# Optimization experiments

Measured on AMD Instinct MI355X. Metric: run time of the kernel, lower is better.

The kernel has to match this reference:

```python
import jax, jax.numpy as jnp
import numpy as np

N_NODES = 50000
N_EDGES = 800000
IN_DIM = 64
HID = 128
NUM_LAYERS = 4
N_GRAPHS = 1024
LEAKY_SLOPE = 0.01


def setup_inputs() -> dict:
    key = jax.random.key(0)
    ks = jax.random.split(key, 16)
    s = 0.05
    inp = {
        "x": jax.random.normal(ks[0], (N_NODES, IN_DIM), dtype=jnp.float32),
        "edge_index": jax.random.randint(ks[1], (2, N_EDGES), 0, N_NODES, dtype=jnp.int64),
        "batch": jnp.sort(jax.random.randint(ks[2], (N_NODES,), 0, N_GRAPHS, dtype=jnp.int64)),
        # layer 0 (in=IN_DIM -> HID, residual projection)
        "l0_W1": jax.random.normal(ks[3], (IN_DIM, HID), dtype=jnp.float32) * s,
        "l0_b1": jnp.zeros((HID,), jnp.float32),
        "l0_W2": jax.random.normal(ks[4], (HID, HID), dtype=jnp.float32) * s,
        "l0_b2": jnp.zeros((HID,), jnp.float32),
        "l0_Wres": jax.random.normal(ks[5], (IN_DIM, HID), dtype=jnp.float32) * s,
        # layers 1..NUM_LAYERS-1 (HID -> HID, identity residual), stacked
        "Ws1": jax.random.normal(ks[6], (NUM_LAYERS - 1, HID, HID), dtype=jnp.float32) * s,
        "bs1": jnp.zeros((NUM_LAYERS - 1, HID), jnp.float32),
        "Ws2": jax.random.normal(ks[7], (NUM_LAYERS - 1, HID, HID), dtype=jnp.float32) * s,
        "bs2": jnp.zeros((NUM_LAYERS - 1, HID), jnp.float32),
        # fc head
        "fW1": jax.random.normal(ks[8], (HID, HID), dtype=jnp.float32) * s,
        "fb1": jnp.zeros((HID,), jnp.float32),
        "fW2": jax.random.normal(ks[9], (HID, 1), dtype=jnp.float32) * s,
        "fb2": jnp.zeros((1,), jnp.float32),
    }
    return inp


def _gin_layer(x, src, dst, W1, b1, W2, b2, res):
    # GIN sum aggregation: gather source node features, scatter-add at targets
    agg = jax.ops.segment_sum(x[src], dst, num_segments=N_NODES)  # [N, d]
    h = x + agg  # (1 + eps) * x + agg, eps = 0
    h = jax.nn.relu(h @ W1 + b1) @ W2 + b2
    return jax.nn.relu(h + res)


def reference(x, edge_index, batch,
              l0_W1, l0_b1, l0_W2, l0_b2, l0_Wres,
              Ws1, bs1, Ws2, bs2,
              fW1, fb1, fW2, fb2):
    src, dst = edge_index[0], edge_index[1]
    # layer 0 with linear residual projection (in_dim != hidden_dim)
    h = _gin_layer(x, src, dst, l0_W1, l0_b1, l0_W2, l0_b2, x @ l0_Wres)
    # remaining layers with identity residual
    for i in range(NUM_LAYERS - 1):
        h = _gin_layer(h, src, dst, Ws1[i], bs1[i], Ws2[i], bs2[i], h)
    # global mean pool over graphs
    sums = jax.ops.segment_sum(h, batch, num_segments=N_GRAPHS)  # [G, HID]
    counts = jax.ops.segment_sum(jnp.ones((h.shape[0],), h.dtype), batch, num_segments=N_GRAPHS)
    pooled = sums / jnp.maximum(counts, 1.0)[:, None]
    # fc head: Linear -> LeakyReLU -> Linear
    out = jax.nn.leaky_relu(pooled @ fW1 + fb1, negative_slope=LEAKY_SLOPE) @ fW2 + fb2
    return out  # [G, 1]
```

## Files before the change

kernel.cpp:

```cpp
#include <hip/hip_runtime.h>

#define NN 50000
#define NE 800000
#define IND 64
#define HID 128
#define NG 1024

#define NBK 391
#define BCAP 2560

typedef short bf16x8 __attribute__((ext_vector_type(8)));
typedef float f32x4 __attribute__((ext_vector_type(4)));

static __device__ __forceinline__ unsigned short f2bf(float f) {
    unsigned int u = __float_as_uint(f);
    return (unsigned short)((u + 0x7FFFu + ((u >> 16) & 1u)) >> 16);
}
static __device__ __forceinline__ float bf2f(unsigned short h) {
    return __uint_as_float(((unsigned int)h) << 16);
}
static __device__ __forceinline__ float4 f4zero() { return make_float4(0.f, 0.f, 0.f, 0.f); }

__global__ void bin_kernel(const int* __restrict__ src, const int* __restrict__ dst,
                           int* __restrict__ bcur, unsigned int* __restrict__ bedge) {
    __shared__ int hist[NBK];
    __shared__ int base[NBK];
    int tid = threadIdx.x;
    for (int i = tid; i < NBK; i += 256) hist[i] = 0;
    __syncthreads();
    int e0 = blockIdx.x * 4096;
    unsigned int pk[16];
    int bk[16], lo[16];
#pragma unroll
    for (int j = 0; j < 16; ++j) {
        int e = e0 + j * 256 + tid;
        bk[j] = -1;
        if (e < NE) {
            int s = src[e], d = dst[e];
            pk[j] = (unsigned int)s | ((unsigned int)d << 16);
            bk[j] = d >> 7;
            lo[j] = atomicAdd(&hist[bk[j]], 1);
        }
    }
    __syncthreads();
    for (int i = tid; i < NBK; i += 256)
        base[i] = hist[i] ? atomicAdd(&bcur[i], hist[i]) : 0;
    __syncthreads();
#pragma unroll
    for (int j = 0; j < 16; ++j) {
        if (bk[j] >= 0) {
            int idx = base[bk[j]] + lo[j];
            if (idx < BCAP) bedge[(size_t)bk[j] * BCAP + idx] = pk[j];
        }
    }
}

__global__ void build_csr_kernel(const unsigned int* __restrict__ bedge,
                                 const int* __restrict__ bcur, int* __restrict__ row_beg,
                                 int* __restrict__ row_end, int* __restrict__ esrc) {
    __shared__ unsigned int se[BCAP];
    __shared__ int h[128], sc[128], cur[128];
    int b = blockIdx.x, tid = threadIdx.x;
    int cnt = min(bcur[b], BCAP);
    for (int i = tid; i < cnt; i += 256) se[i] = bedge[(size_t)b * BCAP + i];
    if (tid < 128) h[tid] = 0;
    __syncthreads();
    for (int i = tid; i < cnt; i += 256) atomicAdd(&h[(se[i] >> 16) & 127], 1);
    __syncthreads();
    if (tid < 128) sc[tid] = h[tid];
    __syncthreads();
    for (int off = 1; off < 128; off <<= 1) {
        int add = 0;
        if (tid < 128 && tid >= off) add = sc[tid - off];
        __syncthreads();
        if (tid < 128) sc[tid] += add;
        __syncthreads();
    }
    if (tid < 128) {
        int ex = sc[tid] - h[tid];
        int n = (b << 7) + tid;
        if (n < NN) {
            row_beg[n] = b * BCAP + ex;
            row_end[n] = b * BCAP + sc[tid];
        }
        cur[tid] = ex;
    }
    __syncthreads();
    for (int i = tid; i < cnt; i += 256) {
        unsigned int v = se[i];
        int dl = (v >> 16) & 127;
        int pos = atomicAdd(&cur[dl], 1);
        esrc[(size_t)b * BCAP + pos] = (int)(v & 0xffffu);
    }
}

__global__ void convert_all(const float* __restrict__ Wres, const float* __restrict__ W1,
                            const float* __restrict__ W2, const float* __restrict__ Ws1,
                            const float* __restrict__ Ws2, short* __restrict__ wresHi,
                            short* __restrict__ wresLo, short* __restrict__ w1Hi,
                            short* __restrict__ w1Lo, short* __restrict__ w2Hi,
                            short* __restrict__ w2Lo, short* __restrict__ ws1Hi,
                            short* __restrict__ ws1Lo, short* __restrict__ ws2Hi,
                            short* __restrict__ ws2Lo) {
    int t = blockIdx.x * 256 + threadIdx.x;
    const float* W;
    short *hi, *lo;
    int K, idx;
    if (t < 8192) { W = Wres; hi = wresHi; lo = wresLo; K = 64; idx = t; }
    else if (t < 16384) { W = W1; hi = w1Hi; lo = w1Lo; K = 64; idx = t - 8192; }
    else if (t < 32768) { W = W2; hi = w2Hi; lo = w2Lo; K = 128; idx = t - 16384; }
    else if (t < 81920) { W = Ws1; hi = ws1Hi; lo = ws1Lo; K = 128; idx = t - 32768; }
    else { W = Ws2; hi = ws2Hi; lo = ws2Lo; K = 128; idx = t - 81920; }
    int m = idx / (K * 128);
    int r = idx - m * K * 128;
    int n = r / K, k = r - n * K;
    float w = W[(size_t)m * K * 128 + k * 128 + n];
    unsigned short hh = f2bf(w);
    hi[idx] = (short)hh;
    lo[idx] = (short)f2bf(w - bf2f(hh));
}

__global__ void to_bf16_kernel(const float* __restrict__ s, short* __restrict__ d, int total) {
    int i = blockIdx.x * 256 + threadIdx.x;
    if (i < total) d[i] = (short)f2bf(s[i]);
}

__global__ void agg128b_kernel(const unsigned int* __restrict__ hb, const float* __restrict__ hf,
                               const int* __restrict__ row_beg, const int* __restrict__ row_end,
                               const int* __restrict__ es, float* __restrict__ t) {
    int wv = threadIdx.x >> 6, lane = threadIdx.x & 63;
    int n = blockIdx.x * 4 + wv;
    if (n >= NN) return;
    int beg = row_beg[n], end = row_end[n];
    float2 acc = ((const float2*)hf)[(size_t)n * 64 + lane];
    int e = beg;
    for (; e + 8 <= end; e += 8) {
        unsigned int v0 = hb[(size_t)es[e] * 64 + lane];
        unsigned int v1 = hb[(size_t)es[e + 1] * 64 + lane];
        unsigned int v2 = hb[(size_t)es[e + 2] * 64 + lane];
        unsigned int v3 = hb[(size_t)es[e + 3] * 64 + lane];
        unsigned int v4 = hb[(size_t)es[e + 4] * 64 + lane];
        unsigned int v5 = hb[(size_t)es[e + 5] * 64 + lane];
        unsigned int v6 = hb[(size_t)es[e + 6] * 64 + lane];
        unsigned int v7 = hb[(size_t)es[e + 7] * 64 + lane];
        acc.x += __uint_as_float(v0 << 16) + __uint_as_float(v1 << 16) +
                 __uint_as_float(v2 << 16) + __uint_as_float(v3 << 16) +
                 __uint_as_float(v4 << 16) + __uint_as_float(v5 << 16) +
                 __uint_as_float(v6 << 16) + __uint_as_float(v7 << 16);
        acc.y += __uint_as_float(v0 & 0xffff0000u) + __uint_as_float(v1 & 0xffff0000u) +
                 __uint_as_float(v2 & 0xffff0000u) + __uint_as_float(v3 & 0xffff0000u) +
                 __uint_as_float(v4 & 0xffff0000u) + __uint_as_float(v5 & 0xffff0000u) +
                 __uint_as_float(v6 & 0xffff0000u) + __uint_as_float(v7 & 0xffff0000u);
    }
    for (; e + 4 <= end; e += 4) {
        unsigned int v0 = hb[(size_t)es[e] * 64 + lane];
        unsigned int v1 = hb[(size_t)es[e + 1] * 64 + lane];
        unsigned int v2 = hb[(size_t)es[e + 2] * 64 + lane];
        unsigned int v3 = hb[(size_t)es[e + 3] * 64 + lane];
        acc.x += __uint_as_float(v0 << 16) + __uint_as_float(v1 << 16) +
                 __uint_as_float(v2 << 16) + __uint_as_float(v3 << 16);
        acc.y += __uint_as_float(v0 & 0xffff0000u) + __uint_as_float(v1 & 0xffff0000u) +
                 __uint_as_float(v2 & 0xffff0000u) + __uint_as_float(v3 & 0xffff0000u);
    }
    for (; e < end; ++e) {
        unsigned int v = hb[(size_t)es[e] * 64 + lane];
        acc.x += __uint_as_float(v << 16);
        acc.y += __uint_as_float(v & 0xffff0000u);
    }
    ((float2*)t)[(size_t)n * 64 + lane] = acc;
}

__global__ void agg64b_kernel(const unsigned short* __restrict__ xb, const float* __restrict__ xf,
                              const int* __restrict__ row_beg, const int* __restrict__ row_end,
                              const int* __restrict__ es, float* __restrict__ t) {
    int wv = threadIdx.x >> 6, lane = threadIdx.x & 63;
    int n = blockIdx.x * 4 + wv;
    if (n >= NN) return;
    int beg = row_beg[n], end = row_end[n];
    float acc = xf[(size_t)n * 64 + lane];
    int e = beg;
    for (; e + 4 <= end; e += 4) {
        int s0 = es[e], s1 = es[e + 1], s2 = es[e + 2], s3 = es[e + 3];
        acc += bf2f(xb[(size_t)s0 * 64 + lane]) + bf2f(xb[(size_t)s1 * 64 + lane]) +
               bf2f(xb[(size_t)s2 * 64 + lane]) + bf2f(xb[(size_t)s3 * 64 + lane]);
    }
    for (; e < end; ++e) acc += bf2f(xb[(size_t)es[e] * 64 + lane]);
    t[(size_t)n * 64 + lane] = acc;
}

__global__ __launch_bounds__(256, 3) void fused2(
    const float* __restrict__ tin, const float* __restrict__ xres,
    const short* __restrict__ W1Hi, const short* __restrict__ W1Lo,
    const float* __restrict__ b1, const short* __restrict__ W2Hi,
    const short* __restrict__ W2Lo, const float* __restrict__ b2,
    float* __restrict__ hout, short* __restrict__ hbout) {
    __shared__ short lds[16384];
    int tid = threadIdx.x;
    int rowBase = blockIdx.x * 64;
    int lane = tid & 63, wv = tid >> 6;
    int m = lane & 15, g = lane >> 4;

    float4 sv[8];
#pragma unroll
    for (int j = 0; j < 8; ++j) {
        int i = j * 256 + tid;
        int r = i >> 5, c4 = i & 31;
        int row = rowBase + r;
        sv[j] = f4zero();
        if (row < NN) sv[j] = ((const float4*)(tin + (size_t)row * 128))[c4];
    }
    bf16x8 wh[2][4], wl[2][4];
#pragma unroll
    for (int ctl = 0; ctl < 2; ++ctl) {
        int col = wv * 32 + ctl * 16 + m;
#pragma unroll
        for (int kc = 0; kc < 4; ++kc) {
            wh[ctl][kc] = *(const bf16x8*)(W1Hi + col * 128 + kc * 32 + g * 8);
            wl[ctl][kc] = *(const bf16x8*)(W1Lo + col * 128 + kc * 32 + g * 8);
        }
    }
#pragma unroll
    for (int j = 0; j < 8; ++j) {
        int i = j * 256 + tid;
        int r = i >> 5, c4 = i & 31;
        float4 v = sv[j];
        unsigned short hx = f2bf(v.x), hy = f2bf(v.y), hz = f2bf(v.z), hw = f2bf(v.w);
        short4 hv = {(short)hx, (short)hy, (short)hz, (short)hw};
        short4 lv = {(short)f2bf(v.x - bf2f(hx)), (short)f2bf(v.y - bf2f(hy)),
                     (short)f2bf(v.z - bf2f(hz)), (short)f2bf(v.w - bf2f(hw))};
        int sidx = (r * 128 + c4 * 4) ^ ((r & 7) << 3);
        *(short4*)(lds + sidx) = hv;
        *(short4*)(lds + 8192 + sidx) = lv;
    }
    __syncthreads();

    f32x4 acc1[4][2];
#pragma unroll
    for (int s = 0; s < 4; ++s) {
        int rloc = s * 16 + m;
        bf16x8 tHi[4], tLo[4];
#pragma unroll
        for (int kc = 0; kc < 4; ++kc) {
            int idx = (rloc * 128 + kc * 32 + g * 8) ^ ((rloc & 7) << 3);
            tHi[kc] = *(const bf16x8*)(lds + idx);
            tLo[kc] = *(const bf16x8*)(lds + 8192 + idx);
        }
#pragma unroll
        for (int ctl = 0; ctl < 2; ++ctl) {
            float bv = b1[wv * 32 + ctl * 16 + m];
            f32x4 a = {bv, bv, bv, bv};
#pragma unroll
            for (int kc = 0; kc < 4; ++kc) {
                a = __builtin_amdgcn_mfma_f32_16x16x32_bf16(tHi[kc], wh[ctl][kc], a, 0, 0, 0);
                a = __builtin_amdgcn_mfma_f32_16x16x32_bf16(tLo[kc], wh[ctl][kc], a, 0, 0, 0);
                a = __builtin_amdgcn_mfma_f32_16x16x32_bf16(tHi[kc], wl[ctl][kc], a, 0, 0, 0);
            }
            acc1[s][ctl] = a;
        }
    }
    __syncthreads();

#pragma unroll
    for (int s = 0; s < 4; ++s) {
#pragma unroll
        for (int ctl = 0; ctl < 2; ++ctl) {
            int col = wv * 32 + ctl * 16 + m;
#pragma unroll
            for (int i = 0; i < 4; ++i) {
                float u = fmaxf(acc1[s][ctl][i], 0.f);
                unsigned short uh = f2bf(u);
                int ru = s * 16 + g * 4 + i;
                int sidx = (ru * 128 + col) ^ ((ru & 7) << 3);
                lds[sidx] = (short)uh;
                lds[8192 + sidx] = (short)f2bf(u - bf2f(uh));
            }
        }
    }
#pragma unroll
    for (int ctl = 0; ctl < 2; ++ctl) {
        int col = wv * 32 + ctl * 16 + m;
#pragma unroll
        for (int kc = 0; kc < 4; ++kc) {
            wh[ctl][kc] = *(const bf16x8*)(W2Hi + col * 128 + kc * 32 + g * 8);
            wl[ctl][kc] = *(const bf16x8*)(W2Lo + col * 128 + kc * 32 + g * 8);
        }
    }
    __syncthreads();

#pragma unroll
    for (int s = 0; s < 4; ++s) {
        int rloc = s * 16 + m;
        bf16x8 uHi[4], uLo[4];
#pragma unroll
        for (int kc = 0; kc < 4; ++kc) {
            int idx = (rloc * 128 + kc * 32 + g * 8) ^ ((rloc & 7) << 3);
            uHi[kc] = *(const bf16x8*)(lds + idx);
            uLo[kc] = *(const bf16x8*)(lds + 8192 + idx);
        }
#pragma unroll
        for (int ctl = 0; ctl < 2; ++ctl) {
            int col = wv * 32 + ctl * 16 + m;
            float bv = b2[col];
            f32x4 a = {bv, bv, bv, bv};
#pragma unroll
            for (int kc = 0; kc < 4; ++kc) {
                a = __builtin_amdgcn_mfma_f32_16x16x32_bf16(uHi[kc], wh[ctl][kc], a, 0, 0, 0);
                a = __builtin_amdgcn_mfma_f32_16x16x32_bf16(uLo[kc], wh[ctl][kc], a, 0, 0, 0);
                a = __builtin_amdgcn_mfma_f32_16x16x32_bf16(uHi[kc], wl[ctl][kc], a, 0, 0, 0);
            }
#pragma unroll
            for (int i = 0; i < 4; ++i) {
                int row = rowBase + s * 16 + g * 4 + i;
                if (row < NN) {
                    float v = fmaxf(a[i] + xres[(size_t)row * 128 + col], 0.f);
                    hout[(size_t)row * 128 + col] = v;
                    hbout[(size_t)row * 128 + col] = (short)f2bf(v);
                }
            }
        }
    }
}

template <int L0>
__global__ __launch_bounds__(256, 4) void fused_layer(
    const float* __restrict__ tin, const float* __restrict__ xres,
    const short* __restrict__ W1Hi, const short* __restrict__ W1Lo,
    const float* __restrict__ b1, const short* __restrict__ W2Hi,
    const short* __restrict__ W2Lo, const float* __restrict__ b2,
    const short* __restrict__ WrHi, const short* __restrict__ WrLo,
    float* __restrict__ hout, short* __restrict__ hbout) {
    constexpr int KIN = L0 ? 64 : 128;
    constexpr int NKC1 = KIN / 32;
    __shared__ short lds[16384];
    int tid = threadIdx.x;
    int rowBase = blockIdx.x * 64;
    int lane = tid & 63, wv = tid >> 6;
    int m = lane & 15, g = lane >> 4;

    for (int i = tid; i < 64 * KIN / 4; i += 256) {
        int r = i / (KIN / 4), c4 = i - r * (KIN / 4);
        int row = rowBase + r;
        float4 v = f4zero();
        if (row < NN) v = ((const float4*)(tin + (size_t)row * KIN))[c4];
        unsigned short hx = f2bf(v.x), hy = f2bf(v.y), hz = f2bf(v.z), hw = f2bf(v.w);
        short4 hv = {(short)hx, (short)hy, (short)hz, (short)hw};
        short4 lv = {(short)f2bf(v.x - bf2f(hx)), (short)f2bf(v.y - bf2f(hy)),
                     (short)f2bf(v.z - bf2f(hz)), (short)f2bf(v.w - bf2f(hw))};
        int sidx = (r * KIN + c4 * 4) ^ ((r & 7) << 3);
        *(short4*)(lds + sidx) = hv;
        *(short4*)(lds + 64 * KIN + sidx) = lv;
    }
    if (L0) {
        for (int i = tid; i < 64 * 64 / 4; i += 256) {
            int r = i >> 4, c4 = i & 15;
            int row = rowBase + r;
            float4 v = f4zero();
            if (row < NN) v = ((const float4*)(xres + (size_t)row * 64))[c4];
            unsigned short hx = f2bf(v.x), hy = f2bf(v.y), hz = f2bf(v.z), hw = f2bf(v.w);
            short4 hv = {(short)hx, (short)hy, (short)hz, (short)hw};
            short4 lv = {(short)f2bf(v.x - bf2f(hx)), (short)f2bf(v.y - bf2f(hy)),
                         (short)f2bf(v.z - bf2f(hz)), (short)f2bf(v.w - bf2f(hw))};
            int sidx = (r * 64 + c4 * 4) ^ ((r & 7) << 3);
            *(short4*)(lds + 8192 + sidx) = hv;
            *(short4*)(lds + 12288 + sidx) = lv;
        }
    }
    __syncthreads();

    int rloc = wv * 16 + m;
    bf16x8 tHi[NKC1], tLo[NKC1];
    bf16x8 xHi[2], xLo[2];
#pragma unroll
    for (int kc = 0; kc < NKC1; ++kc) {
        int idx = (rloc * KIN + kc * 32 + g * 8) ^ ((rloc & 7) << 3);
        tHi[kc] = *(const bf16x8*)(lds + idx);
        tLo[kc] = *(const bf16x8*)(lds + 64 * KIN + idx);
    }
    if (L0) {
#pragma unroll
        for (int kc = 0; kc < 2; ++kc) {
            int idx = (rloc * 64 + kc * 32 + g * 8) ^ ((rloc & 7) << 3);
            xHi[kc] = *(const bf16x8*)(lds + 8192 + idx);
            xLo[kc] = *(const bf16x8*)(lds + 12288 + idx);
        }
    }
    __syncthreads();

    f32x4 racc[8];
#pragma unroll
    for (int ct = 0; ct < 8; ++ct) {
        int col = ct * 16 + m;
        float bv = b1[col];
        f32x4 acc = {bv, bv, bv, bv};
#pragma unroll
        for (int kc = 0; kc < NKC1; ++kc) {
            bf16x8 bhi = *(const bf16x8*)(W1Hi + col * KIN + kc * 32 + g * 8);
            bf16x8 blo = *(const bf16x8*)(W1Lo + col * KIN + kc * 32 + g * 8);
            acc = __builtin_amdgcn_mfma_f32_16x16x32_bf16(tHi[kc], bhi, acc, 0, 0, 0);
            acc = __builtin_amdgcn_mfma_f32_16x16x32_bf16(tLo[kc], bhi, acc, 0, 0, 0);
            acc = __builtin_amdgcn_mfma_f32_16x16x32_bf16(tHi[kc], blo, acc, 0, 0, 0);
        }
        if (L0) {
            f32x4 r = {0.f, 0.f, 0.f, 0.f};
#pragma unroll
            for (int kc = 0; kc < 2; ++kc) {
                bf16x8 bhi = *(const bf16x8*)(WrHi + col * 64 + kc * 32 + g * 8);
                bf16x8 blo = *(const bf16x8*)(WrLo + col * 64 + kc * 32 + g * 8);
                r = __builtin_amdgcn_mfma_f32_16x16x32_bf16(xHi[kc], bhi, r, 0, 0, 0);
                r = __builtin_amdgcn_mfma_f32_16x16x32_bf16(xLo[kc], bhi, r, 0, 0, 0);
                r = __builtin_amdgcn_mfma_f32_16x16x32_bf16(xHi[kc], blo, r, 0, 0, 0);
            }
            racc[ct] = r;
        }
#pragma unroll
        for (int i = 0; i < 4; ++i) {
            float u = fmaxf(acc[i], 0.f);
            unsigned short uh = f2bf(u);
            int ru = wv * 16 + g * 4 + i;
            int sidx = (ru * 128 + col) ^ ((ru & 7) << 3);
            lds[sidx] = (short)uh;
            lds[8192 + sidx] = (short)f2bf(u - bf2f(uh));
        }
    }
    __syncthreads();

    bf16x8 uHi[4], uLo[4];
#pragma unroll
    for (int kc = 0; kc < 4; ++kc) {
        int idx = (rloc * 128 + kc * 32 + g * 8) ^ ((rloc & 7) << 3);
        uHi[kc] = *(const bf16x8*)(lds + idx);
        uLo[kc] = *(const bf16x8*)(lds + 8192 + idx);
    }
    __syncthreads();

    float* fld = (float*)lds;
#pragma unroll
    for (int ct = 0; ct < 8; ++ct) {
        int col = ct * 16 + m;
        float bv = b2[col];
        f32x4 acc = {bv, bv, bv, bv};
#pragma unroll
        for (int kc = 0; kc < 4; ++kc) {
            bf16x8 bhi = *(const bf16x8*)(W2Hi + col * 128 + kc * 32 + g * 8);
            bf16x8 blo = *(const bf16x8*)(W2Lo + col * 128 + kc * 32 + g * 8);
            acc = __builtin_amdgcn_mfma_f32_16x16x32_bf16(uHi[kc], bhi, acc, 0, 0, 0);
            acc = __builtin_amdgcn_mfma_f32_16x16x32_bf16(uLo[kc], bhi, acc, 0, 0, 0);
            acc = __builtin_amdgcn_mfma_f32_16x16x32_bf16(uHi[kc], blo, acc, 0, 0, 0);
        }
#pragma unroll
        for (int i = 0; i < 4; ++i) {
            float v = acc[i];
            if (L0) v = fmaxf(v + racc[ct][i], 0.f);
            int ru = wv * 16 + g * 4 + i;
            int fidx = (ru * 128 + col) ^ ((ru & 7) << 3);
            fld[fidx] = v;
        }
    }
    __syncthreads();

    for (int i = tid; i < 2048; i += 256) {
        int r = i >> 5, c4 = i & 31;
        int row = rowBase + r;
        if (row >= NN) continue;
        int fidx = (r * 128 + c4 * 4) ^ ((r & 7) << 3);
        float4 v = *(const float4*)(fld + fidx);
        if (!L0) {
            float4 rs = ((const float4*)(xres + (size_t)row * 128))[c4];
            v.x = fmaxf(v.x + rs.x, 0.f);
            v.y = fmaxf(v.y + rs.y, 0.f);
            v.z = fmaxf(v.z + rs.z, 0.f);
            v.w = fmaxf(v.w + rs.w, 0.f);
        }
        ((float4*)(hout + (size_t)row * 128))[c4] = v;
        short4 bv4 = {(short)f2bf(v.x), (short)f2bf(v.y), (short)f2bf(v.z), (short)f2bf(v.w)};
        ((short4*)(hbout + (size_t)row * 128))[c4] = bv4;
    }
}

static __device__ __forceinline__ int lbound(const int* __restrict__ a, int n, int v) {
    int lo = 0, hi = n;
    while (lo < hi) {
        int mid = (lo + hi) >> 1;
        if (a[mid] < v) lo = mid + 1;
        else hi = mid;
    }
    return lo;
}

__global__ void head_kernel(const float* __restrict__ h, const int* __restrict__ batch,
                            const float* __restrict__ fW1, const float* __restrict__ fb1,
                            const float* __restrict__ fW2, const float* __restrict__ fb2,
                            float* __restrict__ out) {
    __shared__ float sp[128];
    __shared__ float su[128];
    __shared__ int sr[2];
    int g = blockIdx.x, t = threadIdx.x;
    if (t == 0) sr[0] = lbound(batch, NN, g);
    if (t == 1) sr[1] = lbound(batch, NN, g + 1);
    __syncthreads();
    int beg = sr[0], end = sr[1];
    float acc = 0.f;
    for (int i = beg; i < end; ++i) acc += h[(size_t)i * 128 + t];
    sp[t] = acc / (float)max(end - beg, 1);
    __syncthreads();
    float a = fb1[t];
#pragma unroll 4
    for (int k = 0; k < 128; ++k) a = fmaf(sp[k], fW1[k * 128 + t], a);
    a = a > 0.f ? a : 0.01f * a;
    su[t] = a * fW2[t];
    __syncthreads();
    for (int s2 = 64; s2 > 0; s2 >>= 1) {
        if (t < s2) su[t] += su[t + s2];
        __syncthreads();
    }
    if (t == 0) out[g] = su[0] + fb2[0];
}

extern "C" void kernel_launch(void* const* d_in, const int* in_sizes, int n_in,
                              void* d_out, int out_size, void* d_ws, size_t ws_size,
                              hipStream_t stream) {
    const float* x = (const float*)d_in[0];
    const int* eidx = (const int*)d_in[1];
    const int* src = eidx;
    const int* dst = eidx + NE;
    const int* batch = (const int*)d_in[2];
    const float* l0_W1 = (const float*)d_in[3];
    const float* l0_b1 = (const float*)d_in[4];
    const float* l0_W2 = (const float*)d_in[5];
    const float* l0_b2 = (const float*)d_in[6];
    const float* l0_Wres = (const float*)d_in[7];
    const float* Ws1 = (const float*)d_in[8];
    const float* bs1 = (const float*)d_in[9];
    const float* Ws2 = (const float*)d_in[10];
    const float* bs2 = (const float*)d_in[11];
    const float* fW1 = (const float*)d_in[12];
    const float* fb1 = (const float*)d_in[13];
    const float* fW2 = (const float*)d_in[14];
    const float* fb2 = (const float*)d_in[15];
    float* out = (float*)d_out;

    size_t used = 0;
    auto alloc = [&](size_t bytes) -> char* {
        char* r = (char*)d_ws + used;
        used = (used + bytes + 255) & ~(size_t)255;
        return r;
    };
    float* A = (float*)alloc((size_t)NN * HID * 4);
    float* B = (float*)alloc((size_t)NN * HID * 4);
    float* C = (float*)alloc((size_t)NN * HID * 4);
    int* bcur = (int*)alloc((size_t)NBK * 4);
    int* row_beg = (int*)alloc((size_t)NN * 4);
    int* row_end = (int*)alloc((size_t)NN * 4);
    int* esrc = (int*)alloc((size_t)NBK * BCAP * 4);
    char* shared_region = alloc((size_t)NN * IND * 2 > (size_t)NBK * BCAP * 4
                                    ? (size_t)NN * IND * 2
                                    : (size_t)NBK * BCAP * 4);
    unsigned int* bedge = (unsigned int*)shared_region;
    short* xb = (short*)shared_region;
    short* wresHi = (short*)alloc(128 * 64 * 2);
    short* wresLo = (short*)alloc(128 * 64 * 2);
    short* w1Hi = (short*)alloc(128 * 64 * 2);
    short* w1Lo = (short*)alloc(128 * 64 * 2);
    short* w2Hi = (short*)alloc(128 * 128 * 2);
    short* w2Lo = (short*)alloc(128 * 128 * 2);
    short* ws1Hi = (short*)alloc(3 * 128 * 128 * 2);
    short* ws1Lo = (short*)alloc(3 * 128 * 128 * 2);
    short* ws2Hi = (short*)alloc(3 * 128 * 128 * 2);
    short* ws2Lo = (short*)alloc(3 * 128 * 128 * 2);
    short* hb = (short*)alloc((size_t)NN * HID * 2);

    hipMemsetAsync(bcur, 0, (size_t)NBK * 4, stream);

    const int GB = (NN + 63) / 64;
    const int AGGB = (NN + 3) / 4;

    convert_all<<<512, 256, 0, stream>>>(l0_Wres, l0_W1, l0_W2, Ws1, Ws2, wresHi, wresLo, w1Hi,
                                         w1Lo, w2Hi, w2Lo, ws1Hi, ws1Lo, ws2Hi, ws2Lo);

    bin_kernel<<<(NE + 4095) / 4096, 256, 0, stream>>>(src, dst, bcur, bedge);
    build_csr_kernel<<<NBK, 256, 0, stream>>>(bedge, bcur, row_beg, row_end, esrc);

    to_bf16_kernel<<<(NN * IND + 255) / 256, 256, 0, stream>>>(x, xb, NN * IND);

    agg64b_kernel<<<AGGB, 256, 0, stream>>>((const unsigned short*)xb, x, row_beg, row_end, esrc,
                                            A);
    fused_layer<1><<<GB, 256, 0, stream>>>(A, x, w1Hi, w1Lo, l0_b1, w2Hi, w2Lo, l0_b2, wresHi,
                                           wresLo, B, hb);

    float* hcur = B;
    float* hnxt = C;
    for (int l = 0; l < 3; ++l) {
        agg128b_kernel<<<AGGB, 256, 0, stream>>>((const unsigned int*)hb, hcur, row_beg, row_end,
                                                 esrc, A);
        fused2<<<GB, 256, 0, stream>>>(A, hcur, ws1Hi + (size_t)l * 16384,
                                       ws1Lo + (size_t)l * 16384, bs1 + (size_t)l * HID,
                                       ws2Hi + (size_t)l * 16384, ws2Lo + (size_t)l * 16384,
                                       bs2 + (size_t)l * HID, hnxt, hb);
        float* t2 = hcur;
        hcur = hnxt;
        hnxt = t2;
    }

    head_kernel<<<NG, 128, 0, stream>>>(hcur, batch, fW1, fb1, fW2, fb2, out);
}
```

Measured before the change: 469.4 us.

## Restructure layer-0 fused kernel to keep weights in registers per wave column slice

The templated fused_layer used for layer 0 is replaced by a dedicated fused0 kernel in which each wave owns a 32-column slice and keeps its W1/Wres (then W2) fragments in registers, iterating over all four 16-row subtiles. This mirrors the existing fused2 design. Weights are then loaded once per wave instead of once per column tile per wave, and the separate fp32 LDS staging pass for the output is dropped in favour of direct writes. Global loads for inputs are also issued up front to overlap latency. The cost is higher register pressure (launch bounds lowered to 3) and uncoalesced scalar output stores.

```diff
diff --git a/kernel.cpp b/kernel.cpp
--- a/kernel.cpp
+++ b/kernel.cpp
@@ -321,159 +321,157 @@
     }
 }
 
-template <int L0>
-__global__ __launch_bounds__(256, 4) void fused_layer(
-    const float* __restrict__ tin, const float* __restrict__ xres,
+__global__ __launch_bounds__(256, 3) void fused0(
+    const float* __restrict__ tin, const float* __restrict__ x,
     const short* __restrict__ W1Hi, const short* __restrict__ W1Lo,
     const float* __restrict__ b1, const short* __restrict__ W2Hi,
     const short* __restrict__ W2Lo, const float* __restrict__ b2,
     const short* __restrict__ WrHi, const short* __restrict__ WrLo,
     float* __restrict__ hout, short* __restrict__ hbout) {
-    constexpr int KIN = L0 ? 64 : 128;
-    constexpr int NKC1 = KIN / 32;
     __shared__ short lds[16384];
     int tid = threadIdx.x;
     int rowBase = blockIdx.x * 64;
     int lane = tid & 63, wv = tid >> 6;
     int m = lane & 15, g = lane >> 4;
 
-    for (int i = tid; i < 64 * KIN / 4; i += 256) {
-        int r = i / (KIN / 4), c4 = i - r * (KIN / 4);
+    float4 sv[4], sx[4];
+#pragma unroll
+    for (int j = 0; j < 4; ++j) {
+        int i = j * 256 + tid;
+        int r = i >> 4, c4 = i & 15;
         int row = rowBase + r;
-        float4 v = f4zero();
-        if (row < NN) v = ((const float4*)(tin + (size_t)row * KIN))[c4];
+        sv[j] = f4zero();
+        sx[j] = f4zero();
+        if (row < NN) {
+            sv[j] = ((const float4*)(tin + (size_t)row * 64))[c4];
+            sx[j] = ((const float4*)(x + (size_t)row * 64))[c4];
+        }
+    }
+    bf16x8 wh[2][4], wl[2][4];
+#pragma unroll
+    for (int ctl = 0; ctl < 2; ++ctl) {
+        int col = wv * 32 + ctl * 16 + m;
+#pragma unroll
+        for (int kc = 0; kc < 2; ++kc) {
+            wh[ctl][kc] = *(const bf16x8*)(W1Hi + col * 64 + kc * 32 + g * 8);
+            wl[ctl][kc] = *(const bf16x8*)(W1Lo + col * 64 + kc * 32 + g * 8);
+            wh[ctl][2 + kc] = *(const bf16x8*)(WrHi + col * 64 + kc * 32 + g * 8);
+            wl[ctl][2 + kc] = *(const bf16x8*)(WrLo + col * 64 + kc * 32 + g * 8);
+        }
+    }
+#pragma unroll
+    for (int j = 0; j < 4; ++j) {
+        int i = j * 256 + tid;
+        int r = i >> 4, c4 = i & 15;
+        int sidx = (r * 64 + c4 * 4) ^ ((r & 7) << 3);
+        float4 v = sv[j];
         unsigned short hx = f2bf(v.x), hy = f2bf(v.y), hz = f2bf(v.z), hw = f2bf(v.w);
         short4 hv = {(short)hx, (short)hy, (short)hz, (short)hw};
         short4 lv = {(short)f2bf(v.x - bf2f(hx)), (short)f2bf(v.y - bf2f(hy)),
                      (short)f2bf(v.z - bf2f(hz)), (short)f2bf(v.w - bf2f(hw))};
-        int sidx = (r * KIN + c4 * 4) ^ ((r & 7) << 3);
         *(short4*)(lds + sidx) = hv;
-        *(short4*)(lds + 64 * KIN + sidx) = lv;
-    }
-    if (L0) {
-        for (int i = tid; i < 64 * 64 / 4; i += 256) {
-            int r = i >> 4, c4 = i & 15;
-            int row = rowBase + r;
-            float4 v = f4zero();
-            if (row < NN) v = ((const float4*)(xres + (size_t)row * 64))[c4];
-            unsigned short hx = f2bf(v.x), hy = f2bf(v.y), hz = f2bf(v.z), hw = f2bf(v.w);
-            short4 hv = {(short)hx, (short)hy, (short)hz, (short)hw};
-            short4 lv = {(short)f2bf(v.x - bf2f(hx)), (short)f2bf(v.y - bf2f(hy)),
-                         (short)f2bf(v.z - bf2f(hz)), (short)f2bf(v.w - bf2f(hw))};
-            int sidx = (r * 64 + c4 * 4) ^ ((r & 7) << 3);
-            *(short4*)(lds + 8192 + sidx) = hv;
-            *(short4*)(lds + 12288 + sidx) = lv;
-        }
-    }
-    __syncthreads();
-
-    int rloc = wv * 16 + m;
-    bf16x8 tHi[NKC1], tLo[NKC1];
-    bf16x8 xHi[2], xLo[2];
-#pragma unroll
-    for (int kc = 0; kc < NKC1; ++kc) {
-        int idx = (rloc * KIN + kc * 32 + g * 8) ^ ((rloc & 7) << 3);
-        tHi[kc] = *(const bf16x8*)(lds + idx);
-        tLo[kc] = *(const bf16x8*)(lds + 64 * KIN + idx);
-    }
-    if (L0) {
+        *(short4*)(lds + 4096 + sidx) = lv;
+        v = sx[j];
+        hx = f2bf(v.x), hy = f2bf(v.y), hz = f2bf(v.z), hw = f2bf(v.w);
+        short4 hv2 = {(short)hx, (short)hy, (short)hz, (short)hw};
+        short4 lv2 = {(short)f2bf(v.x - bf2f(hx)), (short)f2bf(v.y - bf2f(hy)),
+                      (short)f2bf(v.z - bf2f(hz)), (short)f2bf(v.w - bf2f(hw))};
+        *(short4*)(lds + 8192 + sidx) = hv2;
+        *(short4*)(lds + 12288 + sidx) = lv2;
+    }
+    __syncthreads();
+
+    f32x4 acc1[4][2], racc[4][2];
+#pragma unroll
+    for (int s = 0; s < 4; ++s) {
+        int rloc = s * 16 + m;
+        bf16x8 tH[2], tL[2], xH[2], xL[2];
 #pragma unroll
         for (int kc = 0; kc < 2; ++kc) {
             int idx = (rloc * 64 + kc * 32 + g * 8) ^ ((rloc & 7) << 3);
-            xHi[kc] = *(const bf16x8*)(lds + 8192 + idx);
-            xLo[kc] = *(const bf16x8*)(lds + 12288 + idx);
-        }
-    }
-    __syncthreads();
-
-    f32x4 racc[8];
-#pragma unroll
-    for (int ct = 0; ct < 8; ++ct) {
-        int col = ct * 16 + m;
-        float bv = b1[col];
-        f32x4 acc = {bv, bv, bv, bv};
-#pragma unroll
-        for (int kc = 0; kc < NKC1; ++kc) {
-            bf16x8 bhi = *(const bf16x8*)(W1Hi + col * KIN + kc * 32 + g * 8);
-            bf16x8 blo = *(const bf16x8*)(W1Lo + col * KIN + kc * 32 + g * 8);
-            acc = __builtin_amdgcn_mfma_f32_16x16x32_bf16(tHi[kc], bhi, acc, 0, 0, 0);
-            acc = __builtin_amdgcn_mfma_f32_16x16x32_bf16(tLo[kc], bhi, acc, 0, 0, 0);
-            acc = __builtin_amdgcn_mfma_f32_16x16x32_bf16(tHi[kc], blo, acc, 0, 0, 0);
-        }
-        if (L0) {
-            f32x4 r = {0.f, 0.f, 0.f, 0.f};
+            tH[kc] = *(const bf16x8*)(lds + idx);
+            tL[kc] = *(const bf16x8*)(lds + 4096 + idx);
+            xH[kc] = *(const bf16x8*)(lds + 8192 + idx);
+            xL[kc] = *(const bf16x8*)(lds + 12288 + idx);
+        }
+#pragma unroll
+        for (int ctl = 0; ctl < 2; ++ctl) {
+            float bv = b1[wv * 32 + ctl * 16 + m];
+            f32x4 a = {bv, bv, bv, bv};
+            f32x4 r4 = {0.f, 0.f, 0.f, 0.f};
 #pragma unroll
             for (int kc = 0; kc < 2; ++kc) {
-                bf16x8 bhi = *(const bf16x8*)(WrHi + col * 64 + kc * 32 + g * 8);
-                bf16x8 blo = *(const bf16x8*)(WrLo + col * 64 + kc * 32 + g * 8);
-                r = __builtin_amdgcn_mfma_f32_16x16x32_bf16(xHi[kc], bhi, r, 0, 0, 0);
-                r = __builtin_amdgcn_mfma_f32_16x16x32_bf16(xLo[kc], bhi, r, 0, 0, 0);
-                r = __builtin_amdgcn_mfma_f32_16x16x32_bf16(xHi[kc], blo, r, 0, 0, 0);
-            }
-            racc[ct] = r;
-        }
-#pragma unroll
-        for (int i = 0; i < 4; ++i) {
-            float u = fmaxf(acc[i], 0.f);
-            unsigned short uh = f2bf(u);
-            int ru = wv * 16 + g * 4 + i;
-            int sidx = (ru * 128 + col) ^ ((ru & 7) << 3);
-            lds[sidx] = (short)uh;
-            lds[8192 + sidx] = (short)f2bf(u - bf2f(uh));
-        }
-    }
-    __syncthreads();
-
-    bf16x8 uHi[4], uLo[4];
-#pragma unroll
-    for (int kc = 0; kc < 4; ++kc) {
-        int idx = (rloc * 128 + kc * 32 + g * 8) ^ ((rloc & 7) << 3);
-        uHi[kc] = *(const bf16x8*)(lds + idx);
-        uLo[kc] = *(const bf16x8*)(lds + 8192 + idx);
-    }
-    __syncthreads();
-
-    float* fld = (float*)lds;
-#pragma unroll
-    for (int ct = 0; ct < 8; ++ct) {
-        int col = ct * 16 + m;
-        float bv = b2[col];
-        f32x4 acc = {bv, bv, bv, bv};
+                a = __builtin_amdgcn_mfma_f32_16x16x32_bf16(tH[kc], wh[ctl][kc], a, 0, 0, 0);
+                a = __builtin_amdgcn_mfma_f32_16x16x32_bf16(tL[kc], wh[ctl][kc], a, 0, 0, 0);
+                a = __builtin_amdgcn_mfma_f32_16x16x32_bf16(tH[kc], wl[ctl][kc], a, 0, 0, 0);
+                r4 = __builtin_amdgcn_mfma_f32_16x16x32_bf16(xH[kc], wh[ctl][2 + kc], r4, 0, 0, 0);
+                r4 = __builtin_amdgcn_mfma_f32_16x16x32_bf16(xL[kc], wh[ctl][2 + kc], r4, 0, 0, 0);
+                r4 = __builtin_amdgcn_mfma_f32_16x16x32_bf16(xH[kc], wl[ctl][2 + kc], r4, 0, 0, 0);
+            }
+            acc1[s][ctl] = a;
+            racc[s][ctl] = r4;
+        }
+    }
+    __syncthreads();
+
+#pragma unroll
+    for (int s = 0; s < 4; ++s) {
+#pragma unroll
+        for (int ctl = 0; ctl < 2; ++ctl) {
+            int col = wv * 32 + ctl * 16 + m;
+#pragma unroll
+            for (int i = 0; i < 4; ++i) {
+                float u = fmaxf(acc1[s][ctl][i], 0.f);
+                unsigned short uh = f2bf(u);
+                int ru = s * 16 + g * 4 + i;
+                int sidx = (ru * 128 + col) ^ ((ru & 7) << 3);
+                lds[sidx] = (short)uh;
+                lds[8192 + sidx] = (short)f2bf(u - bf2f(uh));
+            }
+        }
+    }
+#pragma unroll
+    for (int ctl = 0; ctl < 2; ++ctl) {
+        int col = wv * 32 + ctl * 16 + m;
 #pragma unroll
         for (int kc = 0; kc < 4; ++kc) {
-            bf16x8 bhi = *(const bf16x8*)(W2Hi + col * 128 + kc * 32 + g * 8);
-            bf16x8 blo = *(const bf16x8*)(W2Lo + col * 128 + kc * 32 + g * 8);
-            acc = __builtin_amdgcn_mfma_f32_16x16x32_bf16(uHi[kc], bhi, acc, 0, 0, 0);
-            acc = __builtin_amdgcn_mfma_f32_16x16x32_bf16(uLo[kc], bhi, acc, 0, 0, 0);
-            acc = __builtin_amdgcn_mfma_f32_16x16x32_bf16(uHi[kc], blo, acc, 0, 0, 0);
-        }
-#pragma unroll
-        for (int i = 0; i < 4; ++i) {
-            float v = acc[i];
-            if (L0) v = fmaxf(v + racc[ct][i], 0.f);
-            int ru = wv * 16 + g * 4 + i;
-            int fidx = (ru * 128 + col) ^ ((ru & 7) << 3);
-            fld[fidx] = v;
-        }
-    }
-    __syncthreads();
-
-    for (int i = tid; i < 2048; i += 256) {
-        int r = i >> 5, c4 = i & 31;
-        int row = rowBase + r;
-        if (row >= NN) continue;
-        int fidx = (r * 128 + c4 * 4) ^ ((r & 7) << 3);
-        float4 v = *(const float4*)(fld + fidx);
-        if (!L0) {
-            float4 rs = ((const float4*)(xres + (size_t)row * 128))[c4];
-            v.x = fmaxf(v.x + rs.x, 0.f);
-            v.y = fmaxf(v.y + rs.y, 0.f);
-            v.z = fmaxf(v.z + rs.z, 0.f);
-            v.w = fmaxf(v.w + rs.w, 0.f);
-        }
-        ((float4*)(hout + (size_t)row * 128))[c4] = v;
-        short4 bv4 = {(short)f2bf(v.x), (short)f2bf(v.y), (short)f2bf(v.z), (short)f2bf(v.w)};
-        ((short4*)(hbout + (size_t)row * 128))[c4] = bv4;
+            wh[ctl][kc] = *(const bf16x8*)(W2Hi + col * 128 + kc * 32 + g * 8);
+            wl[ctl][kc] = *(const bf16x8*)(W2Lo + col * 128 + kc * 32 + g * 8);
+        }
+    }
+    __syncthreads();
+
+#pragma unroll
+    for (int s = 0; s < 4; ++s) {
+        int rloc = s * 16 + m;
+        bf16x8 uHi[4], uLo[4];
+#pragma unroll
+        for (int kc = 0; kc < 4; ++kc) {
+            int idx = (rloc * 128 + kc * 32 + g * 8) ^ ((rloc & 7) << 3);
+            uHi[kc] = *(const bf16x8*)(lds + idx);
+            uLo[kc] = *(const bf16x8*)(lds + 8192 + idx);
+        }
+#pragma unroll
+        for (int ctl = 0; ctl < 2; ++ctl) {
+            int col = wv * 32 + ctl * 16 + m;
+            float bv = b2[col];
+            f32x4 a = {bv, bv, bv, bv};
+#pragma unroll
+            for (int kc = 0; kc < 4; ++kc) {
+                a = __builtin_amdgcn_mfma_f32_16x16x32_bf16(uHi[kc], wh[ctl][kc], a, 0, 0, 0);
+                a = __builtin_amdgcn_mfma_f32_16x16x32_bf16(uLo[kc], wh[ctl][kc], a, 0, 0, 0);
+                a = __builtin_amdgcn_mfma_f32_16x16x32_bf16(uHi[kc], wl[ctl][kc], a, 0, 0, 0);
+            }
+#pragma unroll
+            for (int i = 0; i < 4; ++i) {
+                int row = rowBase + s * 16 + g * 4 + i;
+                if (row < NN) {
+                    float v = fmaxf(a[i] + racc[s][ctl][i], 0.f);
+                    hout[(size_t)row * 128 + col] = v;
+                    hbout[(size_t)row * 128 + col] = (short)f2bf(v);
+                }
+            }
+        }
     }
 }
 
@@ -584,8 +582,8 @@
 
     agg64b_kernel<<<AGGB, 256, 0, stream>>>((const unsigned short*)xb, x, row_beg, row_end, esrc,
                                             A);
-    fused_layer<1><<<GB, 256, 0, stream>>>(A, x, w1Hi, w1Lo, l0_b1, w2Hi, w2Lo, l0_b2, wresHi,
-                                           wresLo, B, hb);
+    fused0<<<GB, 256, 0, stream>>>(A, x, w1Hi, w1Lo, l0_b1, w2Hi, w2Lo, l0_b2, wresHi, wresLo, B,
+                                   hb);
 
     float* hcur = B;
     float* hnxt = C;
```

New measurement: 435.2 us. 7.3% less time.
